# Performance work log

Measured on AMD Instinct MI355X. Metric: run time of the kernel, lower is better.

## Reference

```python
import jax, jax.numpy as jnp
import numpy as np

B, T, D, H, G = 32, 1000, 512, 512, 8
LN_EPS = 1e-5


def setup_inputs() -> dict:
    key = jax.random.key(0)
    ks = jax.random.split(key, 6)
    return {
        "x": jax.random.normal(ks[0], (B, T, D), jnp.float32),
        "w_in": jax.random.normal(ks[1], (G, D // G, H // G), jnp.float32) * 0.05,
        "w_rec_W": jax.random.normal(ks[2], (2 * H, H), jnp.float32) * 0.05,
        "u_rec": jax.random.normal(ks[3], (2 * H, H), jnp.float32) * 0.05,
        "ln_gamma": jnp.ones((2 * H,), jnp.float32),
        "ln_beta": jnp.zeros((2 * H,), jnp.float32),
        "w_out": jax.random.normal(ks[4], (G, H // G, D // G), jnp.float32) * 0.05,
    }


def grouped_linear(x, w):
    # x: [B,T,G*I], w: [G,I,Ho] -> [B,T,G*Ho]
    b, t, _ = x.shape
    g, i, ho = w.shape
    y = jnp.einsum('btgi,gih->btgh', x.reshape(b, t, g, i), w)
    return y.reshape(b, t, g * ho)


def layernorm(w, gamma, beta):
    mu = jnp.mean(w, axis=-1, keepdims=True)
    var = jnp.var(w, axis=-1, keepdims=True)
    return (w - mu) * jax.lax.rsqrt(var + LN_EPS) * gamma + beta


def ligru_scan(w, u):
    # w: [B,T,2H] precomputed input projection; u: [2H,H] recurrent weight
    ut = u.T  # [H, 2H]
    h0 = jnp.zeros((w.shape[0], u.shape[1]), w.dtype)

    def step(h, wt):
        gates = wt + h @ ut            # [B, 2H]
        at, zt = jnp.split(gates, 2, axis=1)
        zt = jax.nn.sigmoid(zt)
        hcand = jax.nn.relu(at)        # drop_mask = 1.0 (eval)
        h = zt * h + (1.0 - zt) * hcand
        return h, h

    _, hs = jax.lax.scan(step, h0, jnp.swapaxes(w, 0, 1))  # [T,B,H]
    return jnp.swapaxes(hs, 0, 1)  # [B,T,H]


def reference(x, w_in, w_rec_W, u_rec, ln_gamma, ln_beta, w_out):
    h_in = grouped_linear(x, w_in)              # [B,T,H]
    w = jnp.einsum('bth,gh->btg', h_in, w_rec_W)  # [B,T,2H]
    w = layernorm(w, ln_gamma, ln_beta)
    h = ligru_scan(w, u_rec)                    # [B,T,H]
    return grouped_linear(h, w_out)             # [B,T,D]
```

## Files before the change

kernel.cpp:

```cpp
#include <hip/hip_runtime.h>
#include <cstddef>

#define B_SZ 32
#define T_LEN 1000
#define LN_EPS 1e-5f

typedef short bf16x8 __attribute__((ext_vector_type(8)));
typedef float f32x4 __attribute__((ext_vector_type(4)));

__device__ __forceinline__ unsigned short f2bf(float f) {
    unsigned u = __builtin_bit_cast(unsigned, f);
    u += 0x7FFFu + ((u >> 16) & 1u);
    return (unsigned short)(u >> 16);
}

__global__ __launch_bounds__(256) void kw(const float* __restrict__ w_rec,
                                          unsigned short* __restrict__ wrt) {
    int idx  = blockIdx.x * 256 + threadIdx.x;
    int lane = idx & 63;
    int nt   = (idx >> 6) & 63;
    int kt   = idx >> 12;
    int n    = nt * 16 + (lane & 15);
    int k0   = kt * 32 + (lane >> 4) * 8;
    const float* src = w_rec + (size_t)n * 512 + k0;
    unsigned short* dst = wrt + (size_t)idx * 8;
#pragma unroll
    for (int j = 0; j < 8; ++j) dst[j] = f2bf(src[j]);
}

__global__ __launch_bounds__(256) void k1(const float* __restrict__ x,
                                          const float* __restrict__ w_in,
                                          unsigned short* __restrict__ hin) {
    __shared__ alignas(16) float xt[16][512];
    const int tid  = threadIdx.x;
    const int row0 = blockIdx.x * 16;

    for (int i = tid; i < 16 * 128; i += 256) {
        int rr = i >> 7, c4 = i & 127;
        ((float4*)xt[rr])[c4] =
            ((const float4*)(x + (size_t)(row0 + rr) * 512))[c4];
    }
    __syncthreads();

    for (int q = 0; q < 2; ++q) {
        const int c = tid + (q << 8);
        const int g = c >> 6, o = c & 63;
        const float* wb = w_in + (g << 12) + o;
        float wcol[64];
#pragma unroll
        for (int ii = 0; ii < 64; ++ii) wcol[ii] = wb[ii << 6];
#pragma unroll 4
        for (int rr = 0; rr < 16; ++rr) {
            float acc = 0.f;
#pragma unroll
            for (int ii = 0; ii < 64; ++ii) acc += xt[rr][(g << 6) + ii] * wcol[ii];
            hin[(size_t)(row0 + rr) * 512 + c] = f2bf(acc);
        }
    }
}

#define ALD 536
__global__ __launch_bounds__(256) void k2(const unsigned short* __restrict__ hin,
                                          const unsigned short* __restrict__ wrt,
                                          const float* __restrict__ gamma,
                                          const float* __restrict__ beta,
                                          float* __restrict__ w_pre) {
    __shared__ alignas(16) unsigned short At[32 * ALD];
    __shared__ float redS[4][32];
    __shared__ float redQ[4][32];
    __shared__ float stat[2][32];

    const int tid  = threadIdx.x;
    const int w    = tid >> 6;
    const int l    = tid & 63;
    const int kgrp = l >> 4;
    const int lc   = l & 15;
    const int row0 = blockIdx.x * 32;

    for (int sidx = tid; sidx < 2048; sidx += 256) {
        int r = sidx >> 6, sg = sidx & 63;
        *(bf16x8*)(At + r * ALD + sg * 8) =
            *(const bf16x8*)(hin + (size_t)(row0 + r) * 512 + sg * 8);
    }
    __syncthreads();

    f32x4 acc[2][16];
#pragma unroll
    for (int fr = 0; fr < 2; ++fr)
#pragma unroll
        for (int n = 0; n < 16; ++n) acc[fr][n] = f32x4{0.f, 0.f, 0.f, 0.f};

    for (int kt = 0; kt < 16; ++kt) {
        bf16x8 a0 = *(const bf16x8*)(At + (lc)      * ALD + kt * 32 + kgrp * 8);
        bf16x8 a1 = *(const bf16x8*)(At + (16 + lc) * ALD + kt * 32 + kgrp * 8);
        const unsigned short* bb =
            wrt + (((size_t)kt * 64 + w * 16) * 64 + l) * 8;
#pragma unroll
        for (int ntl = 0; ntl < 16; ++ntl) {
            bf16x8 bf = *(const bf16x8*)(bb + (size_t)ntl * 512);
            acc[0][ntl] = __builtin_amdgcn_mfma_f32_16x16x32_bf16(a0, bf, acc[0][ntl], 0, 0, 0);
            acc[1][ntl] = __builtin_amdgcn_mfma_f32_16x16x32_bf16(a1, bf, acc[1][ntl], 0, 0, 0);
        }
    }

    float sums[2][4] = {{0.f}}, sqs[2][4] = {{0.f}};
#pragma unroll
    for (int fr = 0; fr < 2; ++fr)
#pragma unroll
        for (int ntl = 0; ntl < 16; ++ntl)
#pragma unroll
            for (int r = 0; r < 4; ++r) {
                float v = acc[fr][ntl][r];
                sums[fr][r] += v;
                sqs[fr][r]  += v * v;
            }
#pragma unroll
    for (int off = 1; off < 16; off <<= 1)
#pragma unroll
        for (int fr = 0; fr < 2; ++fr)
#pragma unroll
            for (int r = 0; r < 4; ++r) {
                sums[fr][r] += __shfl_xor(sums[fr][r], off);
                sqs[fr][r]  += __shfl_xor(sqs[fr][r], off);
            }
    if (lc == 0) {
#pragma unroll
        for (int fr = 0; fr < 2; ++fr)
#pragma unroll
            for (int r = 0; r < 4; ++r) {
                redS[w][fr * 16 + kgrp * 4 + r] = sums[fr][r];
                redQ[w][fr * 16 + kgrp * 4 + r] = sqs[fr][r];
            }
    }
    __syncthreads();
    if (tid < 32) {
        float S = redS[0][tid] + redS[1][tid] + redS[2][tid] + redS[3][tid];
        float Q = redQ[0][tid] + redQ[1][tid] + redQ[2][tid] + redQ[3][tid];
        float mu  = S * (1.f / 1024.f);
        float var = Q * (1.f / 1024.f) - mu * mu;
        stat[0][tid] = mu;
        stat[1][tid] = rsqrtf(var + LN_EPS);
    }
    __syncthreads();

#pragma unroll
    for (int ntl = 0; ntl < 16; ++ntl) {
        const int col = (w << 8) + (ntl << 4) + lc;
        const float g = gamma[col], bt = beta[col];
#pragma unroll
        for (int fr = 0; fr < 2; ++fr)
#pragma unroll
            for (int r = 0; r < 4; ++r) {
                const int row = fr * 16 + kgrp * 4 + r;
                const float mu  = stat[0][row];
                const float inv = stat[1][row];
                w_pre[((size_t)(row0 + row) << 10) + col] =
                    (acc[fr][ntl][r] - mu) * inv * g + bt;
            }
    }
}

__global__ __launch_bounds__(1024) void k_scan(const float* __restrict__ w_pre,
                                               const float* __restrict__ u,
                                               float* __restrict__ hs,
                                               unsigned int* hbuf) {
    __shared__ alignas(16) float hsh[512];
    __shared__ float gsum[128];

    const int tid = threadIdx.x;
    const int b   = blockIdx.x & 31;
    const int s   = blockIdx.x >> 5;
    const int J0  = s << 6;
    const int row = tid >> 3;
    const int kk  = tid & 7;
    const int jj  = (row < 64) ? (J0 + row) : (448 + J0 + row);

    float ur[64];
    {
        const float4* up = (const float4*)(u + (size_t)jj * 512 + (kk << 6));
#pragma unroll
        for (int m = 0; m < 16; ++m) {
            float4 v = up[m];
            ur[4 * m + 0] = v.x; ur[4 * m + 1] = v.y;
            ur[4 * m + 2] = v.z; ur[4 * m + 3] = v.w;
        }
    }

    const float* wbase = w_pre + ((size_t)b * T_LEN) * 1024 + jj;
    float* outbase = hs + ((size_t)b * T_LEN) * 512 + J0;
    const char* hb8 = (const char*)hsh;

    float hreg = 0.f;
    float wcur = 0.f;
    if (kk == 0) wcur = wbase[0];

    for (int t = 0; t < T_LEN; ++t) {
        unsigned int* in_w  = hbuf + ((((t & 1) << 5) | b) << 9);
        unsigned int* out_w = hbuf + (((((t + 1) & 1) << 5) | b) << 9);

        float wnext = 0.f;
        if (kk == 0 && t + 1 < T_LEN) wnext = wbase[(size_t)(t + 1) << 10];

        if (tid < 256) {
            const unsigned long long* src = (const unsigned long long*)in_w + tid;
            const unsigned int want = (unsigned)t & 3u;
            unsigned long long v = __hip_atomic_load(src, __ATOMIC_RELAXED,
                                                     __HIP_MEMORY_SCOPE_AGENT);
            while (((unsigned)v & 3u) != want ||
                   ((unsigned)(v >> 32) & 3u) != want) {
                v = __hip_atomic_load(src, __ATOMIC_RELAXED,
                                      __HIP_MEMORY_SCOPE_AGENT);
            }
            int c = tid >> 1;
            int a = (c & ~7) | ((c ^ (c >> 4)) & 7);
            *(unsigned long long*)((char*)hsh + (a << 4) + ((tid & 1) << 3)) = v;
        }
        __syncthreads();

        float a0 = 0.f, a1 = 0.f, a2 = 0.f, a3 = 0.f;
        const int base = kk << 8;
#pragma unroll
        for (int i = 0; i < 16; ++i) {
            int off = base + (((i & 8) | ((i ^ kk) & 7)) << 4);
            float4 hv = *(const float4*)(hb8 + off);
            a0 += ur[4 * i + 0] * hv.x;
            a1 += ur[4 * i + 1] * hv.y;
            a2 += ur[4 * i + 2] * hv.z;
            a3 += ur[4 * i + 3] * hv.w;
        }
        float acc = (a0 + a1) + (a2 + a3);
        acc += __shfl_xor(acc, 1);
        acc += __shfl_xor(acc, 2);
        acc += __shfl_xor(acc, 4);
        if (kk == 0) gsum[row] = acc + wcur;
        __syncthreads();

        if (tid < 64) {
            float a  = gsum[tid];
            float zl = gsum[64 + tid];
            float z  = 1.f / (1.f + __expf(-zl));
            float hn = z * hreg + (1.f - z) * fmaxf(a, 0.f);
            hreg = hn;
            unsigned int bits = (__builtin_bit_cast(unsigned int, hn) & ~3u) |
                                ((unsigned)(t + 1) & 3u);
            __hip_atomic_store(out_w + J0 + tid, bits, __ATOMIC_RELAXED,
                               __HIP_MEMORY_SCOPE_AGENT);
            outbase[((size_t)t << 9) + tid] = hn;
        }
        wcur = wnext;
    }
}

__global__ __launch_bounds__(256) void k_out(const float* __restrict__ w_out,
                                             float* __restrict__ io) {
    __shared__ alignas(16) float ht[8][512];
    const int tid  = threadIdx.x;
    const int row0 = blockIdx.x * 8;

    for (int i = tid; i < 8 * 128; i += 256) {
        int rr = i >> 7, c4 = i & 127;
        ((float4*)ht[rr])[c4] =
            ((const float4*)(io + (size_t)(row0 + rr) * 512))[c4];
    }
    __syncthreads();

    for (int q = 0; q < 2; ++q) {
        const int c = tid + (q << 8);
        const int g = c >> 6, o = c & 63;
        const float* wb = w_out + (g << 12) + o;
        float wcol[64];
#pragma unroll
        for (int ii = 0; ii < 64; ++ii) wcol[ii] = wb[ii << 6];
#pragma unroll 4
        for (int rr = 0; rr < 8; ++rr) {
            float acc = 0.f;
#pragma unroll
            for (int ii = 0; ii < 64; ++ii) acc += ht[rr][(g << 6) + ii] * wcol[ii];
            io[(size_t)(row0 + rr) * 512 + c] = acc;
        }
    }
}

extern "C" void kernel_launch(void* const* d_in, const int* in_sizes, int n_in,
                              void* d_out, int out_size, void* d_ws, size_t ws_size,
                              hipStream_t stream) {
    const float* x      = (const float*)d_in[0];
    const float* w_in   = (const float*)d_in[1];
    const float* w_rec  = (const float*)d_in[2];
    const float* u_rec  = (const float*)d_in[3];
    const float* gamma  = (const float*)d_in[4];
    const float* beta   = (const float*)d_in[5];
    const float* w_out  = (const float*)d_in[6];
    float* out = (float*)d_out;

    float*        w_pre = (float*)d_ws;
    unsigned int* hbuf  = (unsigned int*)(w_pre + (size_t)32 * T_LEN * 1024);

    unsigned short* hin = (unsigned short*)d_out;
    unsigned short* wrt = hin + (size_t)32000 * 512;

    hipLaunchKernelGGL(kw, dim3(256), dim3(256), 0, stream, w_rec, wrt);
    hipLaunchKernelGGL(k1, dim3(2000), dim3(256), 0, stream, x, w_in, hin);
    hipLaunchKernelGGL(k2, dim3(1000), dim3(256), 0, stream,
                       hin, wrt, gamma, beta, w_pre);
    hipMemsetAsync(hbuf, 0, 2 * 32 * 512 * sizeof(unsigned int), stream);
    hipLaunchKernelGGL(k_scan, dim3(256), dim3(1024), 0, stream,
                       w_pre, u_rec, out, hbuf);
    hipLaunchKernelGGL(k_out, dim3(4000), dim3(256), 0, stream, w_out, out);
}
```

Before: 1.907 ms.

## Use bf16 MFMA for output grouped linear and fold prep kernels into k1

Rewrites k_out so that each block converts 32 rows of h to bf16 in shared memory and runs the grouped output projection on MFMA 16x16x32 bf16 instructions, with w_out fragments held in registers. This replaces the scalar fp32 dot-product loop. It also merges the w_rec bf16 transpose kernel and the hbuf memset into k1, removing two launches. The cost is lower precision in the output projection (bf16 inputs) and extra work in the first k1 blocks.

Measured after the change: 1.661 ms. -12.9%, faster.

```diff
diff --git a/kernel.cpp b/kernel.cpp
--- a/kernel.cpp
+++ b/kernel.cpp
@@ -14,26 +14,30 @@
     return (unsigned short)(u >> 16);
 }
 
-__global__ __launch_bounds__(256) void kw(const float* __restrict__ w_rec,
-                                          unsigned short* __restrict__ wrt) {
-    int idx  = blockIdx.x * 256 + threadIdx.x;
-    int lane = idx & 63;
-    int nt   = (idx >> 6) & 63;
-    int kt   = idx >> 12;
-    int n    = nt * 16 + (lane & 15);
-    int k0   = kt * 32 + (lane >> 4) * 8;
-    const float* src = w_rec + (size_t)n * 512 + k0;
-    unsigned short* dst = wrt + (size_t)idx * 8;
-#pragma unroll
-    for (int j = 0; j < 8; ++j) dst[j] = f2bf(src[j]);
-}
-
 __global__ __launch_bounds__(256) void k1(const float* __restrict__ x,
                                           const float* __restrict__ w_in,
-                                          unsigned short* __restrict__ hin) {
+                                          const float* __restrict__ w_rec,
+                                          unsigned short* __restrict__ hin,
+                                          unsigned short* __restrict__ wrt,
+                                          unsigned int* __restrict__ hbuf) {
     __shared__ alignas(16) float xt[16][512];
     const int tid  = threadIdx.x;
+    const int gidx = blockIdx.x * 256 + tid;
     const int row0 = blockIdx.x * 16;
+
+    if (gidx < 2 * 32 * 512) hbuf[gidx] = 0u;
+
+    if (gidx < 65536) {
+        int lane = gidx & 63;
+        int nt   = (gidx >> 6) & 63;
+        int kt   = gidx >> 12;
+        int n    = nt * 16 + (lane & 15);
+        int k0   = kt * 32 + (lane >> 4) * 8;
+        const float* src = w_rec + (size_t)n * 512 + k0;
+        unsigned short* dst = wrt + (size_t)gidx * 8;
+#pragma unroll
+        for (int j = 0; j < 8; ++j) dst[j] = f2bf(src[j]);
+    }
 
     for (int i = tid; i < 16 * 128; i += 256) {
         int rr = i >> 7, c4 = i & 127;
@@ -253,32 +257,76 @@
 
 __global__ __launch_bounds__(256) void k_out(const float* __restrict__ w_out,
                                              float* __restrict__ io) {
-    __shared__ alignas(16) float ht[8][512];
+    __shared__ alignas(16) unsigned short At[32 * ALD];
+
     const int tid  = threadIdx.x;
-    const int row0 = blockIdx.x * 8;
-
-    for (int i = tid; i < 8 * 128; i += 256) {
-        int rr = i >> 7, c4 = i & 127;
-        ((float4*)ht[rr])[c4] =
-            ((const float4*)(io + (size_t)(row0 + rr) * 512))[c4];
-    }
-    __syncthreads();
-
-    for (int q = 0; q < 2; ++q) {
-        const int c = tid + (q << 8);
-        const int g = c >> 6, o = c & 63;
-        const float* wb = w_out + (g << 12) + o;
-        float wcol[64];
-#pragma unroll
-        for (int ii = 0; ii < 64; ++ii) wcol[ii] = wb[ii << 6];
-#pragma unroll 4
-        for (int rr = 0; rr < 8; ++rr) {
-            float acc = 0.f;
-#pragma unroll
-            for (int ii = 0; ii < 64; ++ii) acc += ht[rr][(g << 6) + ii] * wcol[ii];
-            io[(size_t)(row0 + rr) * 512 + c] = acc;
-        }
-    }
+    const int w    = tid >> 6;
+    const int l    = tid & 63;
+    const int kgrp = l >> 4;
+    const int lc   = l & 15;
+    const int row0 = blockIdx.x * 32;
+
+    for (int sidx = tid; sidx < 2048; sidx += 256) {
+        int r = sidx >> 6, c8 = sidx & 63;
+        const float4* src = (const float4*)(io + (size_t)(row0 + r) * 512 + c8 * 8);
+        float4 v0 = src[0], v1 = src[1];
+        unsigned short tmp[8] = {f2bf(v0.x), f2bf(v0.y), f2bf(v0.z), f2bf(v0.w),
+                                 f2bf(v1.x), f2bf(v1.y), f2bf(v1.z), f2bf(v1.w)};
+        *(bf16x8*)(At + r * ALD + c8 * 8) = *(bf16x8*)tmp;
+    }
+    __syncthreads();
+
+    bf16x8 bfr[16];
+#pragma unroll
+    for (int gi = 0; gi < 2; ++gi) {
+        const int g = 2 * w + gi;
+#pragma unroll
+        for (int kt = 0; kt < 2; ++kt) {
+            const float* bsrc = w_out + (g << 12) + (kt * 32 + kgrp * 8) * 64 + lc;
+#pragma unroll
+            for (int nt = 0; nt < 4; ++nt) {
+                unsigned short bw[8];
+#pragma unroll
+                for (int j = 0; j < 8; ++j) bw[j] = f2bf(bsrc[j * 64 + nt * 16]);
+                bfr[(gi * 2 + kt) * 4 + nt] = *(bf16x8*)bw;
+            }
+        }
+    }
+
+    f32x4 acc[2][8];
+#pragma unroll
+    for (int fr = 0; fr < 2; ++fr)
+#pragma unroll
+        for (int n = 0; n < 8; ++n) acc[fr][n] = f32x4{0.f, 0.f, 0.f, 0.f};
+
+#pragma unroll
+    for (int gi = 0; gi < 2; ++gi) {
+        const int g = 2 * w + gi;
+#pragma unroll
+        for (int kt = 0; kt < 2; ++kt) {
+            bf16x8 a0 = *(const bf16x8*)(At + lc        * ALD + g * 64 + kt * 32 + kgrp * 8);
+            bf16x8 a1 = *(const bf16x8*)(At + (16 + lc) * ALD + g * 64 + kt * 32 + kgrp * 8);
+#pragma unroll
+            for (int nt = 0; nt < 4; ++nt) {
+                bf16x8 bf = bfr[(gi * 2 + kt) * 4 + nt];
+                acc[0][gi * 4 + nt] = __builtin_amdgcn_mfma_f32_16x16x32_bf16(a0, bf, acc[0][gi * 4 + nt], 0, 0, 0);
+                acc[1][gi * 4 + nt] = __builtin_amdgcn_mfma_f32_16x16x32_bf16(a1, bf, acc[1][gi * 4 + nt], 0, 0, 0);
+            }
+        }
+    }
+
+#pragma unroll
+    for (int gi = 0; gi < 2; ++gi)
+#pragma unroll
+        for (int nt = 0; nt < 4; ++nt) {
+            const int col = (2 * w + gi) * 64 + nt * 16 + lc;
+#pragma unroll
+            for (int fr = 0; fr < 2; ++fr)
+#pragma unroll
+                for (int r = 0; r < 4; ++r)
+                    io[(size_t)(row0 + fr * 16 + kgrp * 4 + r) * 512 + col] =
+                        acc[fr][gi * 4 + nt][r];
+        }
 }
 
 extern "C" void kernel_launch(void* const* d_in, const int* in_sizes, int n_in,
@@ -299,12 +347,11 @@
     unsigned short* hin = (unsigned short*)d_out;
     unsigned short* wrt = hin + (size_t)32000 * 512;
 
-    hipLaunchKernelGGL(kw, dim3(256), dim3(256), 0, stream, w_rec, wrt);
-    hipLaunchKernelGGL(k1, dim3(2000), dim3(256), 0, stream, x, w_in, hin);
+    hipLaunchKernelGGL(k1, dim3(2000), dim3(256), 0, stream,
+                       x, w_in, w_rec, hin, wrt, hbuf);
     hipLaunchKernelGGL(k2, dim3(1000), dim3(256), 0, stream,
                        hin, wrt, gamma, beta, w_pre);
-    hipMemsetAsync(hbuf, 0, 2 * 32 * 512 * sizeof(unsigned int), stream);
     hipLaunchKernelGGL(k_scan, dim3(256), dim3(1024), 0, stream,
                        w_pre, u_rec, out, hbuf);
-    hipLaunchKernelGGL(k_out, dim3(4000), dim3(256), 0, stream, w_out, out);
-}
+    hipLaunchKernelGGL(k_out, dim3(1000), dim3(256), 0, stream, w_out, out);
+}
```
